# Optimization experiments

Measured on AMD Instinct MI355X. Metric: run time of the kernel, lower is better.

The kernel has to match this reference:

```python
import jax, jax.numpy as jnp
import numpy as np

B, L, E, D, A = 256, 196, 2048, 1024, 512


def setup_inputs() -> dict:
    key = jax.random.key(0)
    ks = jax.random.split(key, 9)
    enc_scale = 1.0 / np.sqrt(E)
    dec_scale = 1.0 / np.sqrt(D)
    att_scale = 1.0 / np.sqrt(A)
    return {
        "encoder_out": jax.random.normal(ks[0], (B, L, E), dtype=jnp.float32),
        "decoder_hidden": jax.random.normal(ks[1], (B, D), dtype=jnp.float32),
        "mask1": jax.random.randint(ks[2], (B, L), 0, 2, dtype=jnp.int32),
        "We": jax.random.uniform(ks[3], (E, A), jnp.float32, -enc_scale, enc_scale),
        "be": jax.random.uniform(ks[4], (A,), jnp.float32, -enc_scale, enc_scale),
        "Wd": jax.random.uniform(ks[5], (D, A), jnp.float32, -dec_scale, dec_scale),
        "bd": jax.random.uniform(ks[6], (A,), jnp.float32, -dec_scale, dec_scale),
        "wf": jax.random.uniform(ks[7], (A,), jnp.float32, -att_scale, att_scale),
        "bf": jax.random.uniform(ks[8], (), jnp.float32, -att_scale, att_scale),
    }


def reference(encoder_out, decoder_hidden, mask1, We, be, Wd, bd, wf, bf):
    # att1: [B, L, A]; att2: [B, A]
    att1 = jnp.einsum('ble,ea->bla', encoder_out, We) + be
    att2 = jnp.einsum('bd,da->ba', decoder_hidden, Wd) + bd
    # scores: [B, L]
    att = jnp.einsum('bla,a->bl', jnp.tanh(att1 + att2[:, None, :]), wf) + bf
    att = jnp.where(mask1 == 0, jnp.float32(-1e9), att)
    alpha = jax.nn.softmax(att, axis=1)
    # weighted sum over regions: [B, E]
    awe = jnp.einsum('ble,bl->be', encoder_out, alpha)
    return (awe, alpha)
```

## Files before the change

### kernel.cpp

```cpp
#include <hip/hip_runtime.h>
#include <hip/hip_bf16.h>


#define B_ 256
#define L_ 196
#define E_ 2048
#define D_ 1024
#define A_ 512
#define M_TOT (B_ * L_)

typedef __attribute__((ext_vector_type(8))) short bf16x8;
typedef __attribute__((ext_vector_type(4))) float f32x4;

static __device__ __forceinline__ unsigned short f2bf(float f) {
    union { float f; unsigned u; } u{f};
    unsigned r = u.u + 0x7fffu + ((u.u >> 16) & 1u);
    return (unsigned short)(r >> 16);
}

__global__ __launch_bounds__(256) void k_wepack(const float* __restrict__ We,
                                                unsigned short* __restrict__ WeP) {
    int i = blockIdx.x * 256 + threadIdx.x;
    int k = i >> 9, n = i & 511;
    WeP[((k >> 5) << 14) + (n << 5) + (k & 31)] = f2bf(We[i]);
}

__global__ __launch_bounds__(256) void k_bias2(const float* __restrict__ dec,
                                               const float* __restrict__ Wd,
                                               const float* __restrict__ be,
                                               const float* __restrict__ bd,
                                               float* __restrict__ bias2) {
    int b = blockIdx.x, t = threadIdx.x;
    __shared__ float ds[D_];
    for (int i = t; i < D_; i += 256) ds[i] = dec[b * D_ + i];
    __syncthreads();
    for (int a0 = 0; a0 < A_; a0 += 256) {
        int a = a0 + t;
        float acc = 0.f;
        #pragma unroll 8
        for (int d = 0; d < D_; d++) acc += ds[d] * Wd[d * A_ + a];
        bias2[b * A_ + a] = acc + be[a] + bd[a];
    }
}

__global__ __launch_bounds__(512) void k_gemm_score(
        const float* __restrict__ enc,
        const unsigned short* __restrict__ WeP,
        const float* __restrict__ bias2,
        const float* __restrict__ wf,
        float* __restrict__ scores) {
    __shared__ __align__(16) unsigned short a_lds[64 * 48];
    __shared__ __align__(16) unsigned short b_lds[512 * 48];
    __shared__ float score_lds[64];

    const int tid = threadIdx.x;
    const int m0 = blockIdx.x * 64;
    const int lane = tid & 63;
    const int wid = tid >> 6;
    const int wm = wid >> 2, wn = wid & 3;
    const int kg = lane >> 4, lr = lane & 15;

    const int ar = tid >> 3;
    const int akc = (tid & 7) << 2;
    const float* aptr = enc + (size_t)(m0 + ar) * E_ + akc;
    const unsigned short* bptr = WeP + ((size_t)tid << 5);

    f32x4 acc[2][8];
    #pragma unroll
    for (int i = 0; i < 2; i++)
        #pragma unroll
        for (int j = 0; j < 8; j++) acc[i][j] = (f32x4){0.f, 0.f, 0.f, 0.f};

    for (int kb = 0; kb < 64; kb++) {
        float4 av = *reinterpret_cast<const float4*>(aptr + kb * 32);
        short4 ap;
        ap.x = (short)f2bf(av.x); ap.y = (short)f2bf(av.y);
        ap.z = (short)f2bf(av.z); ap.w = (short)f2bf(av.w);
        *reinterpret_cast<short4*>(&a_lds[ar * 48 + akc]) = ap;
        const uint4* bsrc = reinterpret_cast<const uint4*>(bptr + ((size_t)kb << 14));
        uint4 b0 = bsrc[0], b1 = bsrc[1], b2 = bsrc[2], b3 = bsrc[3];
        uint4* bdst = reinterpret_cast<uint4*>(&b_lds[tid * 48]);
        bdst[0] = b0; bdst[1] = b1; bdst[2] = b2; bdst[3] = b3;
        __syncthreads();

        bf16x8 af[2];
        #pragma unroll
        for (int i = 0; i < 2; i++)
            af[i] = *reinterpret_cast<const bf16x8*>(
                &a_lds[(wm * 32 + i * 16 + lr) * 48 + kg * 8]);
        bf16x8 bfr[8];
        #pragma unroll
        for (int j = 0; j < 8; j++)
            bfr[j] = *reinterpret_cast<const bf16x8*>(
                &b_lds[(wn * 128 + j * 16 + lr) * 48 + kg * 8]);
        #pragma unroll
        for (int i = 0; i < 2; i++)
            #pragma unroll
            for (int j = 0; j < 8; j++)
                acc[i][j] = __builtin_amdgcn_mfma_f32_16x16x32_bf16(
                    af[i], bfr[j], acc[i][j], 0, 0, 0);
        __syncthreads();
    }

    if (tid < 64) score_lds[tid] = 0.f;
    __syncthreads();
    #pragma unroll
    for (int i = 0; i < 2; i++) {
        #pragma unroll
        for (int r = 0; r < 4; r++) {
            int R = wm * 32 + i * 16 + kg * 4 + r;
            int gm = m0 + R;
            int bg = gm / L_;
            float sum = 0.f;
            #pragma unroll
            for (int j = 0; j < 8; j++) {
                int C = wn * 128 + j * 16 + lr;
                float x = acc[i][j][r] + bias2[bg * A_ + C];
                sum += wf[C] * tanhf(x);
            }
            #pragma unroll
            for (int mk = 1; mk < 16; mk <<= 1) sum += __shfl_xor(sum, mk);
            if (lr == 0) atomicAdd(&score_lds[R], sum);
        }
    }
    __syncthreads();
    if (tid < 64) scores[m0 + tid] = score_lds[tid];
}

__global__ __launch_bounds__(256) void k_softmax(const float* __restrict__ scores,
                                                 const int* __restrict__ mask,
                                                 const float* __restrict__ bfp,
                                                 float* __restrict__ alpha) {
    int b = blockIdx.x, t = threadIdx.x;
    float bfv = bfp[0];
    float v = -INFINITY;
    if (t < L_) v = (mask[b * L_ + t] == 0) ? -1e9f : (scores[b * L_ + t] + bfv);
    __shared__ float redm[4], reds[4];
    float m = v;
    #pragma unroll
    for (int s = 1; s < 64; s <<= 1) m = fmaxf(m, __shfl_xor(m, s));
    int w = t >> 6;
    if ((t & 63) == 0) redm[w] = m;
    __syncthreads();
    m = fmaxf(fmaxf(redm[0], redm[1]), fmaxf(redm[2], redm[3]));
    float e = (t < L_) ? expf(v - m) : 0.f;
    float s = e;
    #pragma unroll
    for (int k = 1; k < 64; k <<= 1) s += __shfl_xor(s, k);
    if ((t & 63) == 0) reds[w] = s;
    __syncthreads();
    s = reds[0] + reds[1] + reds[2] + reds[3];
    if (t < L_) alpha[b * L_ + t] = e / s;
}

__global__ __launch_bounds__(64) void k_awe(const float* __restrict__ enc,
                                            const float* __restrict__ alpha,
                                            float* __restrict__ awe) {
    int b = blockIdx.y, ec = blockIdx.x, t = threadIdx.x;
    __shared__ float al[L_];
    for (int l = t; l < L_; l += 64) al[l] = alpha[b * L_ + l];
    __syncthreads();
    int e0 = (ec << 8) + (t << 2);
    const float* base = enc + (size_t)b * L_ * E_ + e0;
    float4 acc = {0.f, 0.f, 0.f, 0.f};
    #pragma unroll 4
    for (int l = 0; l < L_; l++) {
        float4 v = *reinterpret_cast<const float4*>(base + (size_t)l * E_);
        float a = al[l];
        acc.x += a * v.x; acc.y += a * v.y; acc.z += a * v.z; acc.w += a * v.w;
    }
    *reinterpret_cast<float4*>(awe + b * E_ + e0) = acc;
}

extern "C" void kernel_launch(void* const* d_in, const int* in_sizes, int n_in,
                              void* d_out, int out_size, void* d_ws, size_t ws_size,
                              hipStream_t stream) {
    const float* enc  = (const float*)d_in[0];
    const float* dec  = (const float*)d_in[1];
    const int*   mask = (const int*)d_in[2];
    const float* We   = (const float*)d_in[3];
    const float* be   = (const float*)d_in[4];
    const float* Wd   = (const float*)d_in[5];
    const float* bd   = (const float*)d_in[6];
    const float* wf   = (const float*)d_in[7];
    const float* bf   = (const float*)d_in[8];

    float* awe   = (float*)d_out;
    float* alpha = awe + (size_t)B_ * E_;

    char* ws = (char*)d_ws;
    unsigned short* WeP = (unsigned short*)ws;
    float* bias2  = (float*)(ws + (2u << 20));
    float* scores = (float*)(ws + (2u << 20) + (512u << 10));

    hipLaunchKernelGGL(k_wepack, dim3((E_ * A_) / 256), dim3(256), 0, stream, We, WeP);
    hipLaunchKernelGGL(k_bias2, dim3(B_), dim3(256), 0, stream, dec, Wd, be, bd, bias2);
    hipLaunchKernelGGL(k_gemm_score, dim3(M_TOT / 64), dim3(512), 0, stream,
                       enc, WeP, bias2, wf, scores);
    hipLaunchKernelGGL(k_softmax, dim3(B_), dim3(256), 0, stream, scores, mask, bf, alpha);
    hipLaunchKernelGGL(k_awe, dim3(8, B_), dim3(64), 0, stream, enc, alpha, awe);
}
```

Baseline: 458.9 us.

## Double-buffer GEMM with direct global-to-LDS loads, fast tanh, split-L awe reduction

The score GEMM now double-buffers A and B tiles in LDS and streams the packed We tile straight into LDS with global_load_lds, while the next encoder float4 is prefetched one step ahead. This overlaps loads with MFMA work and drops one barrier per k-step. tanh is replaced by an exp/reciprocal formula, and the awe kernel splits L across four wavefronts with an LDS reduction to raise occupancy and memory parallelism. The risks are LDS bank conflicts, because the 48-element padding is gone, and slightly lower tanh accuracy.

```diff
diff --git a/kernel.cpp b/kernel.cpp
--- a/kernel.cpp
+++ b/kernel.cpp
@@ -16,6 +16,12 @@
     union { float f; unsigned u; } u{f};
     unsigned r = u.u + 0x7fffu + ((u.u >> 16) & 1u);
     return (unsigned short)(r >> 16);
+}
+
+static __device__ __forceinline__ void gload_lds16(const void* g, void* l) {
+    __builtin_amdgcn_global_load_lds(
+        (const __attribute__((address_space(1))) unsigned int*)g,
+        (__attribute__((address_space(3))) unsigned int*)l, 16, 0, 0);
 }
 
 __global__ __launch_bounds__(256) void k_wepack(const float* __restrict__ We,
@@ -49,8 +55,8 @@
         const float* __restrict__ bias2,
         const float* __restrict__ wf,
         float* __restrict__ scores) {
-    __shared__ __align__(16) unsigned short a_lds[64 * 48];
-    __shared__ __align__(16) unsigned short b_lds[512 * 48];
+    __shared__ __align__(16) unsigned short aL[2][64 * 32];
+    __shared__ __align__(16) unsigned short bL[2][512 * 32];
     __shared__ float score_lds[64];
 
     const int tid = threadIdx.x;
@@ -60,10 +66,25 @@
     const int wm = wid >> 2, wn = wid & 3;
     const int kg = lane >> 4, lr = lane & 15;
 
-    const int ar = tid >> 3;
-    const int akc = (tid & 7) << 2;
-    const float* aptr = enc + (size_t)(m0 + ar) * E_ + akc;
-    const unsigned short* bptr = WeP + ((size_t)tid << 5);
+    const int ar = tid >> 3, ak = (tid & 7) << 2;
+    const float* aSrc = enc + (size_t)(m0 + ar) * E_ + ak;
+    unsigned short* aDst[2] = { &aL[0][ar * 32 + ak], &aL[1][ar * 32 + ak] };
+
+    const unsigned short* bSrcLane = WeP + (size_t)(wid * 512 + lane * 8);
+
+    auto stageB = [&](int kb, int buf) {
+        const unsigned short* s = bSrcLane + ((size_t)kb << 14);
+        unsigned short* d = &bL[buf][wid * 512];
+        #pragma unroll
+        for (int i = 0; i < 4; i++)
+            gload_lds16(s + i * 4096, d + i * 4096);
+    };
+    auto writeA = [&](const float4& v, int buf) {
+        short4 p;
+        p.x = (short)f2bf(v.x); p.y = (short)f2bf(v.y);
+        p.z = (short)f2bf(v.z); p.w = (short)f2bf(v.w);
+        *reinterpret_cast<short4*>(aDst[buf]) = p;
+    };
 
     f32x4 acc[2][8];
     #pragma unroll
@@ -71,36 +92,44 @@
         #pragma unroll
         for (int j = 0; j < 8; j++) acc[i][j] = (f32x4){0.f, 0.f, 0.f, 0.f};
 
-    for (int kb = 0; kb < 64; kb++) {
-        float4 av = *reinterpret_cast<const float4*>(aptr + kb * 32);
-        short4 ap;
-        ap.x = (short)f2bf(av.x); ap.y = (short)f2bf(av.y);
-        ap.z = (short)f2bf(av.z); ap.w = (short)f2bf(av.w);
-        *reinterpret_cast<short4*>(&a_lds[ar * 48 + akc]) = ap;
-        const uint4* bsrc = reinterpret_cast<const uint4*>(bptr + ((size_t)kb << 14));
-        uint4 b0 = bsrc[0], b1 = bsrc[1], b2 = bsrc[2], b3 = bsrc[3];
-        uint4* bdst = reinterpret_cast<uint4*>(&b_lds[tid * 48]);
-        bdst[0] = b0; bdst[1] = b1; bdst[2] = b2; bdst[3] = b3;
-        __syncthreads();
-
-        bf16x8 af[2];
+    auto computeTile = [&](int buf) {
+        bf16x8 afr[2];
         #pragma unroll
         for (int i = 0; i < 2; i++)
-            af[i] = *reinterpret_cast<const bf16x8*>(
-                &a_lds[(wm * 32 + i * 16 + lr) * 48 + kg * 8]);
+            afr[i] = *reinterpret_cast<const bf16x8*>(
+                &aL[buf][(wm * 32 + i * 16 + lr) * 32 + kg * 8]);
         bf16x8 bfr[8];
         #pragma unroll
         for (int j = 0; j < 8; j++)
             bfr[j] = *reinterpret_cast<const bf16x8*>(
-                &b_lds[(wn * 128 + j * 16 + lr) * 48 + kg * 8]);
+                &bL[buf][(wn * 128 + j * 16 + lr) * 32 + kg * 8]);
         #pragma unroll
         for (int i = 0; i < 2; i++)
             #pragma unroll
             for (int j = 0; j < 8; j++)
                 acc[i][j] = __builtin_amdgcn_mfma_f32_16x16x32_bf16(
-                    af[i], bfr[j], acc[i][j], 0, 0, 0);
+                    afr[i], bfr[j], acc[i][j], 0, 0, 0);
+    };
+
+    stageB(0, 0);
+    float4 avCur = *reinterpret_cast<const float4*>(aSrc);
+    float4 avHold = *reinterpret_cast<const float4*>(aSrc + 32);
+    writeA(avCur, 0);
+    __syncthreads();
+
+    int buf = 0;
+    for (int t = 0; t < 63; t++) {
+        float4 avNext = avHold;
+        if (t + 2 < 64)
+            avNext = *reinterpret_cast<const float4*>(aSrc + (t + 2) * 32);
+        stageB(t + 1, buf ^ 1);
+        computeTile(buf);
+        writeA(avHold, buf ^ 1);
         __syncthreads();
-    }
+        avHold = avNext;
+        buf ^= 1;
+    }
+    computeTile(buf);
 
     if (tid < 64) score_lds[tid] = 0.f;
     __syncthreads();
@@ -116,7 +145,9 @@
             for (int j = 0; j < 8; j++) {
                 int C = wn * 128 + j * 16 + lr;
                 float x = acc[i][j][r] + bias2[bg * A_ + C];
-                sum += wf[C] * tanhf(x);
+                float ex = __expf(2.f * x);
+                float th = 1.f - 2.f * __builtin_amdgcn_rcpf(ex + 1.f);
+                sum += wf[C] * th;
             }
             #pragma unroll
             for (int mk = 1; mk < 16; mk <<= 1) sum += __shfl_xor(sum, mk);
@@ -153,23 +184,36 @@
     if (t < L_) alpha[b * L_ + t] = e / s;
 }
 
-__global__ __launch_bounds__(64) void k_awe(const float* __restrict__ enc,
-                                            const float* __restrict__ alpha,
-                                            float* __restrict__ awe) {
+__global__ __launch_bounds__(256) void k_awe(const float* __restrict__ enc,
+                                             const float* __restrict__ alpha,
+                                             float* __restrict__ awe) {
     int b = blockIdx.y, ec = blockIdx.x, t = threadIdx.x;
+    int g = t >> 6, lt = t & 63;
     __shared__ float al[L_];
-    for (int l = t; l < L_; l += 64) al[l] = alpha[b * L_ + l];
-    __syncthreads();
-    int e0 = (ec << 8) + (t << 2);
+    __shared__ float4 red[256];
+    if (t < L_) al[t] = alpha[b * L_ + t];
+    __syncthreads();
+    int e0 = (ec << 8) + (lt << 2);
     const float* base = enc + (size_t)b * L_ * E_ + e0;
     float4 acc = {0.f, 0.f, 0.f, 0.f};
-    #pragma unroll 4
-    for (int l = 0; l < L_; l++) {
+    int l0 = g * 49;
+    #pragma unroll 7
+    for (int l = l0; l < l0 + 49; l++) {
         float4 v = *reinterpret_cast<const float4*>(base + (size_t)l * E_);
         float a = al[l];
         acc.x += a * v.x; acc.y += a * v.y; acc.z += a * v.z; acc.w += a * v.w;
     }
-    *reinterpret_cast<float4*>(awe + b * E_ + e0) = acc;
+    red[t] = acc;
+    __syncthreads();
+    if (t < 64) {
+        float4 r0 = red[t], r1 = red[64 + t], r2 = red[128 + t], r3 = red[192 + t];
+        float4 o;
+        o.x = r0.x + r1.x + r2.x + r3.x;
+        o.y = r0.y + r1.y + r2.y + r3.y;
+        o.z = r0.z + r1.z + r2.z + r3.z;
+        o.w = r0.w + r1.w + r2.w + r3.w;
+        *reinterpret_cast<float4*>(awe + b * E_ + (ec << 8) + (t << 2)) = o;
+    }
 }
 
 extern "C" void kernel_launch(void* const* d_in, const int* in_sizes, int n_in,
@@ -198,5 +242,5 @@
     hipLaunchKernelGGL(k_gemm_score, dim3(M_TOT / 64), dim3(512), 0, stream,
                        enc, WeP, bias2, wf, scores);
     hipLaunchKernelGGL(k_softmax, dim3(B_), dim3(256), 0, stream, scores, mask, bf, alpha);
-    hipLaunchKernelGGL(k_awe, dim3(8, B_), dim3(64), 0, stream, enc, alpha, awe);
-}
+    hipLaunchKernelGGL(k_awe, dim3(8, B_), dim3(256), 0, stream, enc, alpha, awe);
+}
```

Measured after the change: 491.5 us. 7.1% more time.
